# Optimization experiments

Measured on AMD Instinct MI355X. Metric: run time of the kernel, lower is better.

The kernel has to match this reference:

```python
import jax, jax.numpy as jnp
import numpy as np

N_HEAD = 16

def setup_inputs() -> dict:
    key = jax.random.key(0)
    k1, k2, k3 = jax.random.split(key, 3)
    B, T, C = 4, 2048, 1024
    x = jax.random.normal(k1, (B, T, C), dtype=jnp.float32)
    W_attn = jax.random.normal(k2, (C, 3 * C), dtype=jnp.float32) * (1.0 / np.sqrt(C))
    W_proj = jax.random.normal(k3, (C, C), dtype=jnp.float32) * (1.0 / np.sqrt(C))
    return {"x": x, "W_attn": W_attn, "W_proj": W_proj}

def reference(x, W_attn, W_proj):
    B, T, C = x.shape
    H = N_HEAD
    D = C // H  # head_dim
    qkv = x @ W_attn                      # (B, T, 3C)
    q, k, v = jnp.split(qkv, 3, axis=-1)
    # (B, T, C) -> (B, H, T, D)
    q = q.reshape(B, T, H, D).transpose(0, 2, 1, 3)
    k = k.reshape(B, T, H, D).transpose(0, 2, 1, 3)
    v = v.reshape(B, T, H, D).transpose(0, 2, 1, 3)
    scale = 1.0 / np.sqrt(D)
    att = jnp.einsum('bhqd,bhkd->bhqk', q, k) * scale  # (B, H, T, T)
    causal = jnp.tril(jnp.ones((T, T), dtype=bool))
    att = jnp.where(causal[None, None, :, :], att, -jnp.inf)
    att = jax.nn.softmax(att, axis=-1)
    y = jnp.einsum('bhqk,bhkd->bhqd', att, v)          # (B, H, T, D)
    y = y.transpose(0, 2, 1, 3).reshape(B, T, C)
    y = y @ W_proj
    return y
```

## Files before the change

### kernel.cpp

```cpp
#include <hip/hip_runtime.h>
#include <hip/hip_bf16.h>
#include <stdint.h>

typedef __attribute__((ext_vector_type(8))) __bf16 bf16x8;
typedef __attribute__((ext_vector_type(4))) __bf16 bf16x4;
typedef __attribute__((ext_vector_type(4))) float f32x4;

static __device__ __forceinline__ ushort f2bf(float f) {
  union { float f; uint32_t u; } v; v.f = f;
  uint32_t u = v.u;
  u += 0x7fffu + ((u >> 16) & 1u);
  return (ushort)(u >> 16);
}

static __device__ __forceinline__ void gl_lds16(const ushort* g, ushort* l) {
  __builtin_amdgcn_global_load_lds(
      (__attribute__((address_space(1))) unsigned int*)(g),
      (__attribute__((address_space(3))) unsigned int*)(l), 16, 0, 0);
}

__global__ __launch_bounds__(256) void cast_f32_bf16(
    const float* __restrict__ in, ushort* __restrict__ out, int n) {
  int i = (blockIdx.x * 256 + threadIdx.x) * 4;
  if (i >= n) return;
  float4 v = *(const float4*)&in[i];
  ushort4 o;
  o.x = f2bf(v.x); o.y = f2bf(v.y); o.z = f2bf(v.z); o.w = f2bf(v.w);
  *(ushort4*)&out[i] = o;
}

__global__ __launch_bounds__(256) void transpose_cast(
    const float* __restrict__ W, ushort* __restrict__ Wt, int K, int N) {
  __shared__ ushort tile[32][33];
  int n0 = blockIdx.x * 32, k0 = blockIdx.y * 32;
  int tx = threadIdx.x, ty = threadIdx.y;
  #pragma unroll
  for (int r = ty; r < 32; r += 8)
    tile[r][tx] = f2bf(W[(size_t)(k0 + r) * N + n0 + tx]);
  __syncthreads();
  #pragma unroll
  for (int r = ty; r < 32; r += 8)
    Wt[(size_t)(n0 + r) * K + k0 + tx] = tile[tx][r];
}

template <int MODE>
__global__ __launch_bounds__(256, 3) void gemm_bt(
    const ushort* __restrict__ A, const ushort* __restrict__ Bt,
    float* __restrict__ Cf, int M, int N, int K,
    ushort* __restrict__ Qo, ushort* __restrict__ Ko, ushort* __restrict__ Vo) {
  __shared__ ushort As[3][128][32];
  __shared__ ushort Bs[3][128][32];
  const int tid = threadIdx.x;
  const int lane = tid & 63;
  const int w = tid >> 6;
  const int wm = (w >> 1) * 64, wn = (w & 1) * 64;
  const int fid = blockIdx.x;
  const int c = fid & 7;
  const int local = fid >> 3;
  const int m0 = (c * 8 + (local & 7)) * 128;
  const int n0 = (local >> 3) * 128;
  const int lr = lane & 15, kg = lane >> 4;
  const int grow = w * 16 + (lane >> 2);
  const int gcol = (lane & 3) * 8;

  auto stage = [&](int buf, int t) {
    const int k0 = t << 5;
    gl_lds16(&A[(size_t)(m0 + grow) * K + k0 + gcol], &As[buf][w * 16][0]);
    gl_lds16(&A[(size_t)(m0 + 64 + grow) * K + k0 + gcol],
             &As[buf][64 + w * 16][0]);
    gl_lds16(&Bt[(size_t)(n0 + grow) * K + k0 + gcol], &Bs[buf][w * 16][0]);
    gl_lds16(&Bt[(size_t)(n0 + 64 + grow) * K + k0 + gcol],
             &Bs[buf][64 + w * 16][0]);
  };

  f32x4 zero = {0.f, 0.f, 0.f, 0.f};
  f32x4 acc[4][4];
  #pragma unroll
  for (int i = 0; i < 4; i++)
    #pragma unroll
    for (int j = 0; j < 4; j++) acc[i][j] = zero;

  const int nsteps = K >> 5;
  stage(0, 0);
  stage(1, 1);
  for (int t = 0; t < nsteps; t++) {
    if (t + 1 < nsteps)
      asm volatile("s_waitcnt vmcnt(4)" ::: "memory");
    else
      asm volatile("s_waitcnt vmcnt(0)" ::: "memory");
    __builtin_amdgcn_s_barrier();
    asm volatile("" ::: "memory");
    if (t + 2 < nsteps) stage((t + 2) % 3, t + 2);
    const ushort(*Ac)[32] = As[t % 3];
    const ushort(*Bc)[32] = Bs[t % 3];
    bf16x8 af[4], bfr[4];
    #pragma unroll
    for (int i = 0; i < 4; i++)
      af[i] = *(const bf16x8*)&Ac[wm + i * 16 + lr][kg * 8];
    #pragma unroll
    for (int j = 0; j < 4; j++)
      bfr[j] = *(const bf16x8*)&Bc[wn + j * 16 + lr][kg * 8];
    __builtin_amdgcn_s_setprio(1);
    #pragma unroll
    for (int i = 0; i < 4; i++)
      #pragma unroll
      for (int j = 0; j < 4; j++)
        acc[i][j] = __builtin_amdgcn_mfma_f32_16x16x32_bf16(af[i], bfr[j],
                                                            acc[i][j], 0, 0, 0);
    __builtin_amdgcn_s_setprio(0);
  }

  #pragma unroll
  for (int i = 0; i < 4; i++) {
    #pragma unroll
    for (int j = 0; j < 4; j++) {
      #pragma unroll
      for (int r = 0; r < 4; r++) {
        int mrow = m0 + wm + i * 16 + kg * 4 + r;
        int ncol = n0 + wn + j * 16 + lr;
        float vv = acc[i][j][r];
        if (MODE == 2) {
          Cf[(size_t)mrow * N + ncol] = vv;
        } else {
          int bb = mrow >> 11, tt = mrow & 2047;
          int which = ncol >> 10, cc = ncol & 1023;
          int hh = cc >> 6, dd = cc & 63;
          size_t bh = (size_t)(bb * 16 + hh);
          if (which == 0) {
            Qo[(bh * 2048 + tt) * 64 + dd] = f2bf(vv * 0.18033688011112042f);
          } else if (which == 1) {
            Ko[(bh * 2048 + tt) * 64 + dd] = f2bf(vv);
          } else {
            Vo[(bh * 64 + dd) * 2048 + tt] = f2bf(vv);
          }
        }
      }
    }
  }
}

__global__ __launch_bounds__(256, 4) void attn_fwd(
    const ushort* __restrict__ Q, const ushort* __restrict__ Kc,
    const ushort* __restrict__ Vt, ushort* __restrict__ Y) {
  __shared__ ushort Ks[2][64][64];
  __shared__ ushort Vs[2][64][64];
  __shared__ ushort Ps[4][16][64];
  const int tid = threadIdx.x;
  const int lane = tid & 63, w = tid >> 6;
  const int lr = lane & 15, kg = lane >> 4;
  int blk = blockIdx.x;
  blk = (blk & 7) * 128 + (blk >> 3);
  const int pair = blk & 15;
  const int bh = blk >> 4;
  const ushort* Qp = Q + (size_t)bh * 2048 * 64;
  const ushort* Kp = Kc + (size_t)bh * 2048 * 64;
  const ushort* Vp = Vt + (size_t)bh * 64 * 2048;
  const int b = bh >> 4, h = bh & 15;
  const int swz = (lr & 14) << 3;
  char* PsB = (char*)&Ps[w][0][0];
  const int srow = lane >> 3, schunk = lane & 7;
  const int cs0 = (kg ^ (lr & 7)) << 3;
  const int cs1 = ((kg ^ 4) ^ (lr & 7)) << 3;
  f32x4 zero = {0.f, 0.f, 0.f, 0.f};

  auto stageKV = [&](int buf, int k0) {
    #pragma unroll
    for (int c = 0; c < 2; c++) {
      const int rbase = w * 16 + c * 8;
      const int r = rbase + srow;
      gl_lds16(&Kp[(size_t)(k0 + r) * 64 + ((schunk ^ (r & 7)) << 3)],
               &Ks[buf][rbase][0]);
      gl_lds16(&Vp[(size_t)r * 2048 + k0 + ((schunk ^ (r & 7)) << 3)],
               &Vs[buf][rbase][0]);
    }
  };

  for (int half = 0; half < 2; half++) {
    const int j = half ? (31 - pair) : pair;
    const int q0b = j << 6;
    const int qw0 = q0b + w * 16;
    bf16x8 qf0 = *(const bf16x8*)&Qp[(size_t)(qw0 + lr) * 64 + kg * 8];
    bf16x8 qf1 = *(const bf16x8*)&Qp[(size_t)(qw0 + lr) * 64 + 32 + kg * 8];
    f32x4 o[4];
    #pragma unroll
    for (int dt = 0; dt < 4; dt++) o[dt] = zero;
    float lsum = 0.f;

    stageKV(0, 0);
    __syncthreads();
    for (int k0 = 0; k0 <= q0b; k0 += 64) {
      const int cur = (k0 >> 6) & 1;
      if (k0 < q0b) stageKV(cur ^ 1, k0 + 64);

      f32x4 s[4];
      #pragma unroll
      for (int ct = 0; ct < 4; ct++) {
        bf16x8 kf0 = *(const bf16x8*)&Ks[cur][ct * 16 + lr][cs0];
        bf16x8 kf1 = *(const bf16x8*)&Ks[cur][ct * 16 + lr][cs1];
        f32x4 z = zero;
        z = __builtin_amdgcn_mfma_f32_16x16x32_bf16(kf0, qf0, z, 0, 0, 0);
        z = __builtin_amdgcn_mfma_f32_16x16x32_bf16(kf1, qf1, z, 0, 0, 0);
        s[ct] = z;
      }
      if (k0 == q0b) {
        const int qrow = qw0 + lr;
        #pragma unroll
        for (int ct = 0; ct < 4; ct++)
          #pragma unroll
          for (int r = 0; r < 4; r++) {
            int kj = k0 + ct * 16 + kg * 4 + r;
            s[ct][r] = (kj > qrow) ? -1e30f : s[ct][r];
          }
      }
      #pragma unroll
      for (int ct = 0; ct < 4; ct++) {
        float p0 = exp2f(s[ct][0]);
        float p1 = exp2f(s[ct][1]);
        float p2 = exp2f(s[ct][2]);
        float p3 = exp2f(s[ct][3]);
        lsum += (p0 + p1) + (p2 + p3);
        bf16x4 pk = {(__bf16)p0, (__bf16)p1, (__bf16)p2, (__bf16)p3};
        *(bf16x4*)(PsB + lr * 128 + ((ct * 32 + kg * 8) ^ swz)) = pk;
      }
      bf16x8 pa0 = *(const bf16x8*)(PsB + lr * 128 + ((kg * 16) ^ swz));
      bf16x8 pa1 = *(const bf16x8*)(PsB + lr * 128 + ((64 + kg * 16) ^ swz));
      #pragma unroll
      for (int dt = 0; dt < 4; dt++) {
        bf16x8 vf0 = *(const bf16x8*)&Vs[cur][dt * 16 + lr][cs0];
        bf16x8 vf1 = *(const bf16x8*)&Vs[cur][dt * 16 + lr][cs1];
        f32x4 t = o[dt];
        t = __builtin_amdgcn_mfma_f32_16x16x32_bf16(pa0, vf0, t, 0, 0, 0);
        t = __builtin_amdgcn_mfma_f32_16x16x32_bf16(pa1, vf1, t, 0, 0, 0);
        o[dt] = t;
      }
      __syncthreads();
    }

    lsum += __shfl_xor(lsum, 16);
    lsum += __shfl_xor(lsum, 32);
    float inv = 1.f / lsum;
    f32x4 ib;
    #pragma unroll
    for (int r = 0; r < 4; r++) ib[r] = __shfl(inv, kg * 4 + r);
    #pragma unroll
    for (int dt = 0; dt < 4; dt++) {
      #pragma unroll
      for (int r = 0; r < 4; r++) {
        size_t t = (size_t)qw0 + kg * 4 + r;
        Y[((size_t)b * 2048 + t) * 1024 + h * 64 + dt * 16 + lr] =
            f2bf(o[dt][r] * ib[r]);
      }
    }
  }
}

extern "C" void kernel_launch(void* const* d_in, const int* in_sizes, int n_in,
                              void* d_out, int out_size, void* d_ws,
                              size_t ws_size, hipStream_t stream) {
  const float* x = (const float*)d_in[0];
  const float* Wa = (const float*)d_in[1];
  const float* Wp = (const float*)d_in[2];
  float* out = (float*)d_out;

  char* ws = (char*)d_ws;
  size_t off = 0;
  auto carve = [&](size_t bytes) {
    void* p = ws + off;
    off += (bytes + 255) & ~(size_t)255;
    return p;
  };
  ushort* Xb = (ushort*)carve(8192ull * 1024 * 2);
  ushort* Wat = (ushort*)carve(3072ull * 1024 * 2);
  ushort* Wpt = (ushort*)carve(1024ull * 1024 * 2);
  ushort* Qh = (ushort*)carve(64ull * 2048 * 64 * 2);
  ushort* Kh = (ushort*)carve(64ull * 2048 * 64 * 2);
  ushort* Vt = (ushort*)carve(64ull * 64 * 2048 * 2);
  ushort* Yb = (ushort*)carve(8192ull * 1024 * 2);

  cast_f32_bf16<<<8192, 256, 0, stream>>>(x, Xb, 8192 * 1024);
  transpose_cast<<<dim3(96, 32), dim3(32, 8), 0, stream>>>(Wa, Wat, 1024, 3072);
  transpose_cast<<<dim3(32, 32), dim3(32, 8), 0, stream>>>(Wp, Wpt, 1024, 1024);
  gemm_bt<1><<<1536, 256, 0, stream>>>(Xb, Wat, nullptr, 8192, 3072, 1024, Qh,
                                       Kh, Vt);
  attn_fwd<<<1024, 256, 0, stream>>>(Qh, Kh, Vt, Yb);
  gemm_bt<2><<<512, 256, 0, stream>>>(Yb, Wpt, out, 8192, 1024, 1024, nullptr,
                                      nullptr, nullptr);
}
```

Baseline: 190.6 us.

## Rewrite GEMM with 256x128 tiles, 8 waves, swizzled LDS and staged epilogue

The bf16 GEMM kernel now uses 512-thread blocks computing 256x128 tiles with BK=64, double-buffered LDS with an XOR swizzle, and interleaves loads of the next tile with four MFMA phases per k-step. The QKV epilogue now goes through LDS so that Q/K/V are written with 16-byte coalesced stores, including the transposed V layout. The aim is more data reuse per tile, fewer LDS bank conflicts and far fewer scattered 2-byte global stores. In exchange it adds more barriers per k-step and higher register and LDS pressure.

```diff
diff --git a/kernel.cpp b/kernel.cpp
--- a/kernel.cpp
+++ b/kernel.cpp
@@ -44,96 +44,175 @@
 }
 
 template <int MODE>
-__global__ __launch_bounds__(256, 3) void gemm_bt(
+__global__ __launch_bounds__(512, 2) void gemm_bt(
     const ushort* __restrict__ A, const ushort* __restrict__ Bt,
     float* __restrict__ Cf, int M, int N, int K,
     ushort* __restrict__ Qo, ushort* __restrict__ Ko, ushort* __restrict__ Vo) {
-  __shared__ ushort As[3][128][32];
-  __shared__ ushort Bs[3][128][32];
+  __shared__ ushort smem[49152];
   const int tid = threadIdx.x;
   const int lane = tid & 63;
   const int w = tid >> 6;
-  const int wm = (w >> 1) * 64, wn = (w & 1) * 64;
+  const int wm = (w >> 2) * 128;
+  const int wn = (w & 3) * 32;
+  const int lr = lane & 15, kg = lane >> 4;
   const int fid = blockIdx.x;
-  const int c = fid & 7;
-  const int local = fid >> 3;
-  const int m0 = (c * 8 + (local & 7)) * 128;
-  const int n0 = (local >> 3) * 128;
-  const int lr = lane & 15, kg = lane >> 4;
-  const int grow = w * 16 + (lane >> 2);
-  const int gcol = (lane & 3) * 8;
-
-  auto stage = [&](int buf, int t) {
-    const int k0 = t << 5;
-    gl_lds16(&A[(size_t)(m0 + grow) * K + k0 + gcol], &As[buf][w * 16][0]);
-    gl_lds16(&A[(size_t)(m0 + 64 + grow) * K + k0 + gcol],
-             &As[buf][64 + w * 16][0]);
-    gl_lds16(&Bt[(size_t)(n0 + grow) * K + k0 + gcol], &Bs[buf][w * 16][0]);
-    gl_lds16(&Bt[(size_t)(n0 + 64 + grow) * K + k0 + gcol],
-             &Bs[buf][64 + w * 16][0]);
+  const int m0 = (((fid & 7) << 2) + ((fid >> 3) & 3)) << 8;
+  const int n0 = (fid >> 5) << 7;
+
+  auto stageA = [&](int buf, int tile, int q) {
+    const int k0 = tile << 6;
+    const int rowb = q * 32 + (w >> 2) * 128 + (w & 3) * 8;
+    gl_lds16(&A[(size_t)(m0 + rowb + (lane >> 3)) * K + k0 +
+                (((lane & 7) ^ (lane >> 3)) << 3)],
+             &smem[buf * 16384 + rowb * 64]);
   };
+  auto stageB = [&](int buf, int tile, int h) {
+    const int k0 = tile << 6;
+    const int rowb = h * 64 + w * 8;
+    gl_lds16(&Bt[(size_t)(n0 + rowb + (lane >> 3)) * K + k0 +
+                 (((lane & 7) ^ (lane >> 3)) << 3)],
+             &smem[32768 + buf * 8192 + rowb * 64]);
+  };
 
   f32x4 zero = {0.f, 0.f, 0.f, 0.f};
-  f32x4 acc[4][4];
+  f32x4 acc[8][2];
   #pragma unroll
-  for (int i = 0; i < 4; i++)
-    #pragma unroll
-    for (int j = 0; j < 4; j++) acc[i][j] = zero;
-
-  const int nsteps = K >> 5;
-  stage(0, 0);
-  stage(1, 1);
-  for (int t = 0; t < nsteps; t++) {
-    if (t + 1 < nsteps)
-      asm volatile("s_waitcnt vmcnt(4)" ::: "memory");
+  for (int i = 0; i < 8; i++)
+    #pragma unroll
+    for (int j = 0; j < 2; j++) acc[i][j] = zero;
+
+  const int cs0 = ((kg ^ (lr & 7)) << 3);
+  const int cs1 = (((4 + kg) ^ (lr & 7)) << 3);
+
+  const int nt = K >> 6;
+  stageA(0, 0, 0); stageA(0, 0, 1); stageA(0, 0, 2); stageA(0, 0, 3);
+  stageB(0, 0, 0); stageB(0, 0, 1);
+  stageA(1, 1, 0); stageA(1, 1, 1); stageA(1, 1, 2);
+  stageB(1, 1, 0); stageB(1, 1, 1);
+
+  for (int t = 0; t < nt; ++t) {
+    const int cur = t & 1, nxt = cur ^ 1;
+    const int ab = cur * 16384, bb = 32768 + cur * 8192;
+    if (t + 1 < nt)
+      asm volatile("s_waitcnt vmcnt(5)" ::: "memory");
     else
       asm volatile("s_waitcnt vmcnt(0)" ::: "memory");
     __builtin_amdgcn_s_barrier();
     asm volatile("" ::: "memory");
-    if (t + 2 < nsteps) stage((t + 2) % 3, t + 2);
-    const ushort(*Ac)[32] = As[t % 3];
-    const ushort(*Bc)[32] = Bs[t % 3];
-    bf16x8 af[4], bfr[4];
-    #pragma unroll
-    for (int i = 0; i < 4; i++)
-      af[i] = *(const bf16x8*)&Ac[wm + i * 16 + lr][kg * 8];
-    #pragma unroll
-    for (int j = 0; j < 4; j++)
-      bfr[j] = *(const bf16x8*)&Bc[wn + j * 16 + lr][kg * 8];
+    if (t + 1 < nt) stageA(nxt, t + 1, 3);
+    bf16x8 bfr[2][2], af[2][2];
+    #pragma unroll
+    for (int j = 0; j < 2; ++j) {
+      const int R = wn + j * 16 + lr;
+      bfr[j][0] = *(const bf16x8*)&smem[bb + R * 64 + cs0];
+      bfr[j][1] = *(const bf16x8*)&smem[bb + R * 64 + cs1];
+    }
+    #pragma unroll
+    for (int il = 0; il < 2; ++il) {
+      const int R = wm + il * 16 + lr;
+      af[il][0] = *(const bf16x8*)&smem[ab + R * 64 + cs0];
+      af[il][1] = *(const bf16x8*)&smem[ab + R * 64 + cs1];
+    }
+    asm volatile("s_waitcnt lgkmcnt(0)" ::: "memory");
+    __builtin_amdgcn_sched_barrier(0);
     __builtin_amdgcn_s_setprio(1);
     #pragma unroll
-    for (int i = 0; i < 4; i++)
-      #pragma unroll
-      for (int j = 0; j < 4; j++)
-        acc[i][j] = __builtin_amdgcn_mfma_f32_16x16x32_bf16(af[i], bfr[j],
-                                                            acc[i][j], 0, 0, 0);
+    for (int il = 0; il < 2; ++il)
+      #pragma unroll
+      for (int j = 0; j < 2; ++j) {
+        acc[il][j] = __builtin_amdgcn_mfma_f32_16x16x32_bf16(
+            af[il][0], bfr[j][0], acc[il][j], 0, 0, 0);
+        acc[il][j] = __builtin_amdgcn_mfma_f32_16x16x32_bf16(
+            af[il][1], bfr[j][1], acc[il][j], 0, 0, 0);
+      }
     __builtin_amdgcn_s_setprio(0);
+    __builtin_amdgcn_s_barrier();
+    asm volatile("" ::: "memory");
+    #pragma unroll
+    for (int p = 1; p < 4; ++p) {
+      if (t + 2 < nt) {
+        stageA(cur, t + 2, p - 1);
+        if (p < 3) stageB(cur, t + 2, p - 1);
+      }
+      bf16x8 a2[2][2];
+      #pragma unroll
+      for (int il = 0; il < 2; ++il) {
+        const int R = wm + (2 * p + il) * 16 + lr;
+        a2[il][0] = *(const bf16x8*)&smem[ab + R * 64 + cs0];
+        a2[il][1] = *(const bf16x8*)&smem[ab + R * 64 + cs1];
+      }
+      asm volatile("s_waitcnt lgkmcnt(0)" ::: "memory");
+      __builtin_amdgcn_sched_barrier(0);
+      __builtin_amdgcn_s_setprio(1);
+      #pragma unroll
+      for (int il = 0; il < 2; ++il)
+        #pragma unroll
+        for (int j = 0; j < 2; ++j) {
+          acc[2 * p + il][j] = __builtin_amdgcn_mfma_f32_16x16x32_bf16(
+              a2[il][0], bfr[j][0], acc[2 * p + il][j], 0, 0, 0);
+          acc[2 * p + il][j] = __builtin_amdgcn_mfma_f32_16x16x32_bf16(
+              a2[il][1], bfr[j][1], acc[2 * p + il][j], 0, 0, 0);
+        }
+      __builtin_amdgcn_s_setprio(0);
+      __builtin_amdgcn_s_barrier();
+      asm volatile("" ::: "memory");
+    }
   }
 
-  #pragma unroll
-  for (int i = 0; i < 4; i++) {
-    #pragma unroll
-    for (int j = 0; j < 4; j++) {
-      #pragma unroll
-      for (int r = 0; r < 4; r++) {
-        int mrow = m0 + wm + i * 16 + kg * 4 + r;
-        int ncol = n0 + wn + j * 16 + lr;
-        float vv = acc[i][j][r];
-        if (MODE == 2) {
-          Cf[(size_t)mrow * N + ncol] = vv;
-        } else {
-          int bb = mrow >> 11, tt = mrow & 2047;
-          int which = ncol >> 10, cc = ncol & 1023;
-          int hh = cc >> 6, dd = cc & 63;
-          size_t bh = (size_t)(bb * 16 + hh);
-          if (which == 0) {
-            Qo[(bh * 2048 + tt) * 64 + dd] = f2bf(vv * 0.18033688011112042f);
-          } else if (which == 1) {
-            Ko[(bh * 2048 + tt) * 64 + dd] = f2bf(vv);
-          } else {
-            Vo[(bh * 64 + dd) * 2048 + tt] = f2bf(vv);
-          }
+  if (MODE == 2) {
+    #pragma unroll
+    for (int i = 0; i < 8; i++)
+      #pragma unroll
+      for (int j = 0; j < 2; j++)
+        #pragma unroll
+        for (int r = 0; r < 4; r++) {
+          int mrow = m0 + wm + i * 16 + kg * 4 + r;
+          int ncol = n0 + wn + j * 16 + lr;
+          Cf[(size_t)mrow * N + ncol] = acc[i][j][r];
         }
+  } else {
+    __syncthreads();
+    ushort* Ls = smem + w * 5120;
+    const int nb = n0 + wn;
+    const int which = nb >> 10;
+    const int bb2 = (m0 + wm) >> 11;
+    const int hh = (nb & 1023) >> 6;
+    const int d0 = nb & 63;
+    const size_t bh = (size_t)(bb2 * 16 + hh);
+    const int t0 = (m0 + wm) & 2047;
+    if (which == 2) {
+      #pragma unroll
+      for (int i = 0; i < 8; i++)
+        #pragma unroll
+        for (int j = 0; j < 2; j++)
+          #pragma unroll
+          for (int r = 0; r < 4; r++)
+            Ls[(j * 16 + lr) * 136 + (i * 16 + kg * 4 + r)] =
+                f2bf(acc[i][j][r]);
+      #pragma unroll
+      for (int it = 0; it < 8; it++) {
+        const int cid = it * 64 + lane;
+        const int d = cid >> 4, chk = cid & 15;
+        bf16x8 v = *(const bf16x8*)&Ls[d * 136 + chk * 8];
+        *(bf16x8*)&Vo[(bh * 64 + d0 + d) * 2048 + t0 + chk * 8] = v;
+      }
+    } else {
+      const float sc = (which == 0) ? 0.18033688011112042f : 1.0f;
+      #pragma unroll
+      for (int i = 0; i < 8; i++)
+        #pragma unroll
+        for (int j = 0; j < 2; j++)
+          #pragma unroll
+          for (int r = 0; r < 4; r++)
+            Ls[(i * 16 + kg * 4 + r) * 40 + (j * 16 + lr)] =
+                f2bf(acc[i][j][r] * sc);
+      ushort* dst = (which == 0) ? Qo : Ko;
+      #pragma unroll
+      for (int it = 0; it < 8; it++) {
+        const int cid = it * 64 + lane;
+        const int row = cid >> 2, chk = cid & 3;
+        bf16x8 v = *(const bf16x8*)&Ls[row * 40 + chk * 8];
+        *(bf16x8*)&dst[(bh * 2048 + t0 + row) * 64 + d0 + chk * 8] = v;
       }
     }
   }
@@ -280,9 +359,9 @@
   cast_f32_bf16<<<8192, 256, 0, stream>>>(x, Xb, 8192 * 1024);
   transpose_cast<<<dim3(96, 32), dim3(32, 8), 0, stream>>>(Wa, Wat, 1024, 3072);
   transpose_cast<<<dim3(32, 32), dim3(32, 8), 0, stream>>>(Wp, Wpt, 1024, 1024);
-  gemm_bt<1><<<1536, 256, 0, stream>>>(Xb, Wat, nullptr, 8192, 3072, 1024, Qh,
-                                       Kh, Vt);
+  gemm_bt<1><<<768, 512, 0, stream>>>(Xb, Wat, nullptr, 8192, 3072, 1024, Qh,
+                                      Kh, Vt);
   attn_fwd<<<1024, 256, 0, stream>>>(Qh, Kh, Vt, Yb);
-  gemm_bt<2><<<512, 256, 0, stream>>>(Yb, Wpt, out, 8192, 1024, 1024, nullptr,
+  gemm_bt<2><<<256, 512, 0, stream>>>(Yb, Wpt, out, 8192, 1024, 1024, nullptr,
                                       nullptr, nullptr);
 }
```

After: 177.0 us. 1.08x faster.
